# Optimization experiments

Measured on AMD Instinct MI355X. Metric: run time of the kernel, lower is better.

The kernel has to match this reference:

```python
import jax, jax.numpy as jnp
import numpy as np
import math

NUM_Q_HEADS = 32
NUM_KV_HEADS = 8


def setup_inputs() -> dict:
    key = jax.random.key(0)
    k1, k2, k3 = jax.random.split(key, 3)
    B, S, E = 2, 2048, 2048
    kv_E = NUM_KV_HEADS * (E // NUM_Q_HEADS)  # 512
    q = jax.random.normal(k1, (B, S, E), dtype=jnp.float32)
    k = jax.random.normal(k2, (B, S, kv_E), dtype=jnp.float32)
    v = jax.random.normal(k3, (B, S, kv_E), dtype=jnp.float32)
    return {"q": q, "k": k, "v": v}


def reference(q, k, v):
    B, S, E = q.shape
    H, KV = NUM_Q_HEADS, NUM_KV_HEADS
    D = E // H
    G = H // KV  # query heads per kv head
    scale = math.sqrt(D)
    # q heads laid out so group g of kv-head h corresponds to q-head h*G+g,
    # matching torch repeat_interleave semantics.
    qh = q.reshape(B, S, KV, G, D).transpose(0, 2, 3, 1, 4)  # [B,KV,G,S,D]
    kh = k.reshape(B, S, KV, D).transpose(0, 2, 1, 3)        # [B,KV,S,D]
    vh = v.reshape(B, S, KV, D).transpose(0, 2, 1, 3)        # [B,KV,S,D]
    scores = jnp.einsum('bkgsd,bktd->bkgst', qh, kh) / scale  # [B,KV,G,S,S]
    weights = jax.nn.softmax(scores, axis=-1)
    out = jnp.einsum('bkgst,bktd->bkgsd', weights, vh)        # [B,KV,G,S,D]
    # back to [B,S,E] with head order (kv_head, group) == q-head index
    return out.transpose(0, 3, 1, 2, 4).reshape(B, S, E)
```

## Files before the change

### kernel.cpp

```cpp
#include <hip/hip_runtime.h>
#include <hip/hip_bf16.h>


#define S_LEN 2048
#define E_DIM 2048
#define KV_E  512
#define D_HEAD 64
#define BN 64
#define NTILE (S_LEN / BN)

typedef __attribute__((ext_vector_type(8))) short short8;
typedef __attribute__((ext_vector_type(4))) float floatx4;
typedef __attribute__((ext_vector_type(4))) unsigned int uint4v;

__device__ __forceinline__ int swb(int r) { return (r & 7) ^ ((r >> 3) & 7); }
__device__ __forceinline__ int sw(int row, int col) {
    return (row << 6) + (col ^ (swb(row) << 3));
}
__device__ __forceinline__ int gKf(int r) { return (r & 3) | (((r >> 3) & 1) << 2); }

__device__ __forceinline__ short bf(float x) {
    return __builtin_bit_cast(short, __float2bfloat16(x));
}
__device__ __forceinline__ unsigned cvtpk(float lo, float hi) {
    unsigned r;
    asm("v_cvt_pk_bf16_f32 %0, %1, %2" : "=v"(r) : "v"(lo), "v"(hi));
    return r;
}

__global__ __launch_bounds__(256)
void gqa_prepack_kernel(const float* __restrict__ k, const float* __restrict__ v,
                        short* __restrict__ ws) {
    __shared__ float vt[BN][D_HEAD + 1];
    const int kt = blockIdx.x, kvh = blockIdx.y, b = blockIdx.z;
    const int tid = threadIdx.x;
    short* wt = ws + ((size_t)(b * 8 + kvh) * NTILE + kt) * 8192;
    const float* kb = k + ((size_t)(b * S_LEN + kt * BN)) * KV_E + kvh * D_HEAD;
    const float* vb = v + ((size_t)(b * S_LEN + kt * BN)) * KV_E + kvh * D_HEAD;

    #pragma unroll
    for (int i = tid; i < 1024; i += 256) {
        const int r = i >> 4, c0 = (i & 15) << 2;
        floatx4 val = *((const floatx4*)(vb + (size_t)r * KV_E + c0));
        vt[r][c0] = val[0]; vt[r][c0 + 1] = val[1];
        vt[r][c0 + 2] = val[2]; vt[r][c0 + 3] = val[3];
    }
    #pragma unroll
    for (int i = tid; i < 512; i += 256) {
        const int o = i << 3;
        const int r = o >> 6;
        const int c = (o & 63) ^ (gKf(r) << 3);
        const float* kp = kb + (size_t)r * KV_E + c;
        floatx4 a  = *((const floatx4*)kp);
        floatx4 b2 = *((const floatx4*)(kp + 4));
        short8 s;
        s[0] = bf(a[0]);  s[1] = bf(a[1]);  s[2] = bf(a[2]);  s[3] = bf(a[3]);
        s[4] = bf(b2[0]); s[5] = bf(b2[1]); s[6] = bf(b2[2]); s[7] = bf(b2[3]);
        *((short8*)(wt + o)) = s;
    }
    __syncthreads();
    #pragma unroll
    for (int i = tid; i < 512; i += 256) {
        const int o = i << 3;
        const int d  = o >> 6;
        const int kk = (o & 63) ^ (swb(d) << 3);
        short8 s;
        #pragma unroll
        for (int j = 0; j < 8; ++j) s[j] = bf(vt[kk + j][d]);
        *((short8*)(wt + 4096 + o)) = s;
    }
}

__global__ __launch_bounds__(256, 4)
void GroupedQueryAttention_36163624632989_kernel(
        const float* __restrict__ q,
        const short* __restrict__ ws,
        float* __restrict__ out, const int B) {
    __shared__ short lds[2 * 8192];

    const int f = blockIdx.x;
    const int chunk = gridDim.x >> 3;
    const int wg = (f & 7) * chunk + (f >> 3);
    const int qt = wg & 31;
    const int t2 = wg >> 5;
    const int b  = t2 % B;
    const int hp = t2 / B;
    const int kvh = hp >> 1;

    const int tid  = threadIdx.x;
    const int w    = tid >> 6;
    const int lane = tid & 63;
    const int quad = lane >> 4;
    const int lc   = lane & 15;

    const int h = (hp << 1) + (w & 1);
    const int rowhalf = w >> 1;

    const float SCL = 1.4426950408889634f / 8.0f;

    const int rowKbase = ((lc >> 2) << 3) + (lc & 3);
    const int gK = gKf(rowKbase);

    short8 aq[2][2];
    #pragma unroll
    for (int mt = 0; mt < 2; ++mt) {
        const int qrow = qt * 64 + rowhalf * 32 + mt * 16 + lc;
        const float* qp = q + ((size_t)(b * S_LEN + qrow)) * E_DIM + h * D_HEAD;
        #pragma unroll
        for (int ks = 0; ks < 2; ++ks) {
            const float* p = qp + ks * 32 + quad * 8;
            floatx4 qa = *((const floatx4*)p);
            floatx4 qb = *((const floatx4*)(p + 4));
            aq[mt][ks][0] = bf(qa[0] * SCL); aq[mt][ks][1] = bf(qa[1] * SCL);
            aq[mt][ks][2] = bf(qa[2] * SCL); aq[mt][ks][3] = bf(qa[3] * SCL);
            aq[mt][ks][4] = bf(qb[0] * SCL); aq[mt][ks][5] = bf(qb[1] * SCL);
            aq[mt][ks][6] = bf(qb[2] * SCL); aq[mt][ks][7] = bf(qb[3] * SCL);
        }
    }

    floatx4 o_acc[2][4];
    float l_r[2] = {0.f, 0.f};
    #pragma unroll
    for (int mt = 0; mt < 2; ++mt)
        #pragma unroll
        for (int i = 0; i < 4; ++i)
            o_acc[mt][i] = (floatx4){0.f, 0.f, 0.f, 0.f};

    const short* wsT = ws + (size_t)(b * 8 + kvh) * NTILE * 8192;

    auto stage = [&](int buf, int kt) {
        const short* src = wsT + (size_t)kt * 8192 + w * 2048 + (lane << 3);
        short* dst = lds + buf * 8192 + w * 2048;
        #pragma unroll
        for (int i = 0; i < 4; ++i)
            __builtin_amdgcn_global_load_lds(
                (const __attribute__((address_space(1))) void*)(src + i * 512),
                (__attribute__((address_space(3))) void*)(dst + i * 512),
                16, 0, 0);
    };

    stage(0, 0);
    __syncthreads();
    int cur = 0;

    for (int kt = 0; kt < NTILE; ++kt) {
        if (kt + 1 < NTILE) stage(cur ^ 1, kt + 1);

        const short* Kt = lds + cur * 8192;
        const short* Vt = Kt + 4096;

        floatx4 accT[2][4];
        #pragma unroll
        for (int mt = 0; mt < 2; ++mt)
            #pragma unroll
            for (int t = 0; t < 4; ++t)
                accT[mt][t] = (floatx4){0.f, 0.f, 0.f, 0.f};
        #pragma unroll
        for (int ks = 0; ks < 2; ++ks) {
            short8 bk4[4];
            #pragma unroll
            for (int t = 0; t < 4; ++t) {
                const int rowK = rowKbase + ((t & 1) << 2) + ((t >> 1) << 5);
                bk4[t] = *((const short8*)(
                    &Kt[(rowK << 6) + ((ks * 32 + quad * 8) ^ (gK << 3))]));
            }
            __builtin_amdgcn_s_setprio(1);
            #pragma unroll
            for (int mt = 0; mt < 2; ++mt)
                #pragma unroll
                for (int t = 0; t < 4; ++t)
                    accT[mt][t] = __builtin_amdgcn_mfma_f32_16x16x32_bf16(
                        bk4[t], aq[mt][ks], accT[mt][t], 0, 0, 0);
            __builtin_amdgcn_s_setprio(0);
        }

        #pragma unroll
        for (int ks = 0; ks < 2; ++ks) {
            short8 bv4[4];
            #pragma unroll
            for (int nt = 0; nt < 4; ++nt)
                bv4[nt] = *((const short8*)(&Vt[sw(nt * 16 + lc, ks * 32 + quad * 8)]));
            #pragma unroll
            for (int mt = 0; mt < 2; ++mt) {
                float e0[4], e1[4];
                #pragma unroll
                for (int r = 0; r < 4; ++r) {
                    e0[r] = exp2f(accT[mt][2 * ks][r]);
                    e1[r] = exp2f(accT[mt][2 * ks + 1][r]);
                    l_r[mt] += e0[r] + e1[r];
                }
                const unsigned a0 = cvtpk(e0[0], e0[1]);
                const unsigned a1 = cvtpk(e0[2], e0[3]);
                const unsigned a2 = cvtpk(e1[0], e1[1]);
                const unsigned a3 = cvtpk(e1[2], e1[3]);
                const short8 ap = __builtin_bit_cast(short8, (uint4v){a0, a1, a2, a3});
                __builtin_amdgcn_s_setprio(1);
                #pragma unroll
                for (int nt = 0; nt < 4; ++nt)
                    o_acc[mt][nt] = __builtin_amdgcn_mfma_f32_16x16x32_bf16(
                        ap, bv4[nt], o_acc[mt][nt], 0, 0, 0);
                __builtin_amdgcn_s_setprio(0);
            }
        }

        __syncthreads();
        cur ^= 1;
    }

    #pragma unroll
    for (int mt = 0; mt < 2; ++mt) {
        float s = l_r[mt];
        s += __shfl_xor(s, 16, 64);
        s += __shfl_xor(s, 32, 64);
        float inv_l[4];
        #pragma unroll
        for (int r = 0; r < 4; ++r)
            inv_l[r] = 1.0f / __shfl(s, quad * 4 + r, 64);
        float* op = out + (size_t)b * S_LEN * E_DIM + h * D_HEAD;
        #pragma unroll
        for (int nt = 0; nt < 4; ++nt) {
            #pragma unroll
            for (int r = 0; r < 4; ++r) {
                const int grow = qt * 64 + rowhalf * 32 + mt * 16 + quad * 4 + r;
                op[(size_t)grow * E_DIM + nt * 16 + lc] = o_acc[mt][nt][r] * inv_l[r];
            }
        }
    }
}

extern "C" void kernel_launch(void* const* d_in, const int* in_sizes, int n_in,
                              void* d_out, int out_size, void* d_ws, size_t ws_size,
                              hipStream_t stream) {
    const float* q = (const float*)d_in[0];
    const float* k = (const float*)d_in[1];
    const float* v = (const float*)d_in[2];
    float* out = (float*)d_out;
    short* ws = (short*)d_ws;
    const int B = in_sizes[0] / (S_LEN * E_DIM);

    dim3 pgrid(NTILE, 8, B);
    gqa_prepack_kernel<<<pgrid, 256, 0, stream>>>(k, v, ws);

    dim3 grid(B * 512);
    GroupedQueryAttention_36163624632989_kernel<<<grid, 256, 0, stream>>>(q, ws, out, B);
}
```

Measured before the change: 187.2 us.

## Prepack K/V tiles in MFMA fragment order and use raw v_exp_f32

The prepack kernel now writes each K and V tile into the workspace in the exact per-lane fragment order that the MFMA operands expect. The attention loop can then read each fragment as a contiguous lane-strided 16-byte LDS load, with no swizzle index arithmetic. Separately, exp2f is replaced by the raw v_exp_f32 instruction, which skips the library's denormal and range handling. In exchange, the prepack does more scattered LDS reads, and exp results may differ for extreme inputs.

```diff
diff --git a/kernel.cpp b/kernel.cpp
--- a/kernel.cpp
+++ b/kernel.cpp
@@ -13,12 +13,6 @@
 typedef __attribute__((ext_vector_type(4))) float floatx4;
 typedef __attribute__((ext_vector_type(4))) unsigned int uint4v;
 
-__device__ __forceinline__ int swb(int r) { return (r & 7) ^ ((r >> 3) & 7); }
-__device__ __forceinline__ int sw(int row, int col) {
-    return (row << 6) + (col ^ (swb(row) << 3));
-}
-__device__ __forceinline__ int gKf(int r) { return (r & 3) | (((r >> 3) & 1) << 2); }
-
 __device__ __forceinline__ short bf(float x) {
     return __builtin_bit_cast(short, __float2bfloat16(x));
 }
@@ -27,11 +21,17 @@
     asm("v_cvt_pk_bf16_f32 %0, %1, %2" : "=v"(r) : "v"(lo), "v"(hi));
     return r;
 }
+__device__ __forceinline__ float vexp2(float x) {
+    float r;
+    asm("v_exp_f32 %0, %1" : "=v"(r) : "v"(x));
+    return r;
+}
 
 __global__ __launch_bounds__(256)
 void gqa_prepack_kernel(const float* __restrict__ k, const float* __restrict__ v,
                         short* __restrict__ ws) {
-    __shared__ float vt[BN][D_HEAD + 1];
+    __shared__ float kf[BN][D_HEAD + 2];
+    __shared__ float vf[BN][D_HEAD + 2];
     const int kt = blockIdx.x, kvh = blockIdx.y, b = blockIdx.z;
     const int tid = threadIdx.x;
     short* wt = ws + ((size_t)(b * 8 + kvh) * NTILE + kt) * 8192;
@@ -41,33 +41,30 @@
     #pragma unroll
     for (int i = tid; i < 1024; i += 256) {
         const int r = i >> 4, c0 = (i & 15) << 2;
-        floatx4 val = *((const floatx4*)(vb + (size_t)r * KV_E + c0));
-        vt[r][c0] = val[0]; vt[r][c0 + 1] = val[1];
-        vt[r][c0 + 2] = val[2]; vt[r][c0 + 3] = val[3];
-    }
-    #pragma unroll
-    for (int i = tid; i < 512; i += 256) {
-        const int o = i << 3;
-        const int r = o >> 6;
-        const int c = (o & 63) ^ (gKf(r) << 3);
-        const float* kp = kb + (size_t)r * KV_E + c;
-        floatx4 a  = *((const floatx4*)kp);
-        floatx4 b2 = *((const floatx4*)(kp + 4));
+        floatx4 k4 = *((const floatx4*)(kb + (size_t)r * KV_E + c0));
+        floatx4 v4 = *((const floatx4*)(vb + (size_t)r * KV_E + c0));
+        kf[r][c0] = k4[0]; kf[r][c0 + 1] = k4[1]; kf[r][c0 + 2] = k4[2]; kf[r][c0 + 3] = k4[3];
+        vf[r][c0] = v4[0]; vf[r][c0 + 1] = v4[1]; vf[r][c0 + 2] = v4[2]; vf[r][c0 + 3] = v4[3];
+    }
+    __syncthreads();
+    #pragma unroll
+    for (int c = tid; c < 1024; c += 256) {
+        const int fk = c >> 6, l = c & 63;
+        const int quad = l >> 4, lc = l & 15;
+        const int ks = (fk >> 2) & 1, sub = fk & 3;
         short8 s;
-        s[0] = bf(a[0]);  s[1] = bf(a[1]);  s[2] = bf(a[2]);  s[3] = bf(a[3]);
-        s[4] = bf(b2[0]); s[5] = bf(b2[1]); s[6] = bf(b2[2]); s[7] = bf(b2[3]);
-        *((short8*)(wt + o)) = s;
-    }
-    __syncthreads();
-    #pragma unroll
-    for (int i = tid; i < 512; i += 256) {
-        const int o = i << 3;
-        const int d  = o >> 6;
-        const int kk = (o & 63) ^ (swb(d) << 3);
-        short8 s;
-        #pragma unroll
-        for (int j = 0; j < 8; ++j) s[j] = bf(vt[kk + j][d]);
-        *((short8*)(wt + 4096 + o)) = s;
+        if (fk < 8) {
+            const int row = ((lc >> 2) << 3) + (lc & 3) + ((sub & 1) << 2) + ((sub >> 1) << 5);
+            const int c0 = ks * 32 + quad * 8;
+            #pragma unroll
+            for (int j = 0; j < 8; ++j) s[j] = bf(kf[row][c0 + j]);
+        } else {
+            const int d = sub * 16 + lc;
+            const int k0 = ks * 32 + quad * 8;
+            #pragma unroll
+            for (int j = 0; j < 8; ++j) s[j] = bf(vf[k0 + j][d]);
+        }
+        *((short8*)(wt + c * 8)) = s;
     }
 }
 
@@ -98,9 +95,6 @@
 
     const float SCL = 1.4426950408889634f / 8.0f;
 
-    const int rowKbase = ((lc >> 2) << 3) + (lc & 3);
-    const int gK = gKf(rowKbase);
-
     short8 aq[2][2];
     #pragma unroll
     for (int mt = 0; mt < 2; ++mt) {
@@ -146,8 +140,7 @@
     for (int kt = 0; kt < NTILE; ++kt) {
         if (kt + 1 < NTILE) stage(cur ^ 1, kt + 1);
 
-        const short* Kt = lds + cur * 8192;
-        const short* Vt = Kt + 4096;
+        const short* fb = lds + cur * 8192 + (lane << 3);
 
         floatx4 accT[2][4];
         #pragma unroll
@@ -159,11 +152,8 @@
         for (int ks = 0; ks < 2; ++ks) {
             short8 bk4[4];
             #pragma unroll
-            for (int t = 0; t < 4; ++t) {
-                const int rowK = rowKbase + ((t & 1) << 2) + ((t >> 1) << 5);
-                bk4[t] = *((const short8*)(
-                    &Kt[(rowK << 6) + ((ks * 32 + quad * 8) ^ (gK << 3))]));
-            }
+            for (int t = 0; t < 4; ++t)
+                bk4[t] = *((const short8*)(fb + (ks * 4 + t) * 512));
             __builtin_amdgcn_s_setprio(1);
             #pragma unroll
             for (int mt = 0; mt < 2; ++mt)
@@ -179,14 +169,14 @@
             short8 bv4[4];
             #pragma unroll
             for (int nt = 0; nt < 4; ++nt)
-                bv4[nt] = *((const short8*)(&Vt[sw(nt * 16 + lc, ks * 32 + quad * 8)]));
+                bv4[nt] = *((const short8*)(fb + (8 + ks * 4 + nt) * 512));
             #pragma unroll
             for (int mt = 0; mt < 2; ++mt) {
                 float e0[4], e1[4];
                 #pragma unroll
                 for (int r = 0; r < 4; ++r) {
-                    e0[r] = exp2f(accT[mt][2 * ks][r]);
-                    e1[r] = exp2f(accT[mt][2 * ks + 1][r]);
+                    e0[r] = vexp2(accT[mt][2 * ks][r]);
+                    e1[r] = vexp2(accT[mt][2 * ks + 1][r]);
                     l_r[mt] += e0[r] + e1[r];
                 }
                 const unsigned a0 = cvtpk(e0[0], e0[1]);
```

Result: faster. 158.1 us (-15.6%).
